# Kernel tuning notes

Measured on AMD Instinct MI355X. Metric: run time of the kernel, lower is better.

The kernel has to match this reference:

```python
import jax, jax.numpy as jnp
import numpy as np

# Grid of blocks: blocks[i][j] is Linear(D, D) if mask[i, j] else None.
N_OUT, N_IN, D, B = 8, 8, 128, 32768
BAND = 2  # active blocks: j <= i and i - j <= BAND


def setup_inputs() -> dict:
    key = jax.random.key(0)
    k1, k2, k3 = jax.random.split(key, 3)
    # X: (num input blocks, batch, block feature dim)
    X = jax.random.normal(k1, (N_IN, B, D), dtype=jnp.float32)
    # W[i, j]: torch.nn.Linear weight of block (i, j), shape (out, in)
    W = jax.random.normal(k2, (N_OUT, N_IN, D, D), dtype=jnp.float32) / np.sqrt(D).astype(np.float32)
    b = jax.random.normal(k3, (N_OUT, N_IN, D), dtype=jnp.float32) * 0.01
    i = jnp.arange(N_OUT)[:, None]
    j = jnp.arange(N_IN)[None, :]
    mask = (j <= i) & (i - j <= BAND)  # banded lower-triangular block sparsity
    return {"X": X, "W": W, "b": b, "mask": mask}


def reference(X, W, b, mask):
    # Sequential2D forward: out[i] = sum_j (X[j] @ W[i,j].T + b[i,j]) over active blocks.
    # None blocks contribute a zero vector, which we express by zeroing masked weights/biases.
    m = mask.astype(W.dtype)                       # (i, j)
    Wm = W * m[:, :, None, None]                   # zero out None blocks
    out = jnp.einsum('jbd,ijod->ibo', X, Wm)       # block-row summation of Linear outputs
    bias = jnp.sum(b * m[:, :, None], axis=1)      # (i, o): sum of active biases per row
    return out + bias[:, None, :]                  # (num_out_blocks, batch, block_out)
```

## Files before the change

kernel.cpp:

```cpp
#include <hip/hip_runtime.h>


#define NOUT  8
#define NIN   8
#define DD    128
#define BATCH 32768
#define BAND  2

#define BM    128
#define WROWS 32
#define SKW   136

typedef __attribute__((ext_vector_type(8))) short  short8;
typedef __attribute__((ext_vector_type(4))) float  floatx4;

__device__ __forceinline__ unsigned short f2bf(float f) {
    unsigned int u = __float_as_uint(f);
    u += 0x7fffu + ((u >> 16) & 1u);
    return (unsigned short)(u >> 16);
}

__device__ __forceinline__ short8 pack8(floatx4 f0, floatx4 f1) {
    short8 p;
    p[0] = (short)f2bf(f0[0]); p[1] = (short)f2bf(f0[1]);
    p[2] = (short)f2bf(f0[2]); p[3] = (short)f2bf(f0[3]);
    p[4] = (short)f2bf(f1[0]); p[5] = (short)f2bf(f1[1]);
    p[6] = (short)f2bf(f1[2]); p[7] = (short)f2bf(f1[3]);
    return p;
}

__global__ __launch_bounds__(256, 2)
void seq2d_kernel(const float* __restrict__ X,
                  const float* __restrict__ W,
                  const float* __restrict__ Bv,
                  float* __restrict__ out) {
    const int i  = blockIdx.y;
    const int m0 = blockIdx.x * BM;

    __shared__ unsigned short sW[DD * SKW];
    __shared__ float sbias[DD];

    const int tid  = threadIdx.x;
    const int lane = tid & 63;
    const int wave = tid >> 6;
    const int l15  = lane & 15;
    const int quad = lane >> 4;
    const int wrow = wave * WROWS;

    int jlo = i - BAND; if (jlo < 0) jlo = 0;
    const int ncs = (i - jlo + 1) * 4;

    const float* xb = X + (size_t)(m0 + wrow + l15) * DD + quad * 8;

    floatx4 px[4][2][2];

    auto prefetch = [&](int slot, int c) {
        const int j  = jlo + (c >> 2);
        const int k0 = (c & 3) * 32;
        const float* p = xb + (size_t)j * (BATCH * DD) + k0;
        px[slot][0][0] = *(const floatx4*)(p);
        px[slot][0][1] = *(const floatx4*)(p + 4);
        px[slot][1][0] = *(const floatx4*)(p + 16 * DD);
        px[slot][1][1] = *(const floatx4*)(p + 16 * DD + 4);
    };

    prefetch(0, 0);
    prefetch(1, 1);
    prefetch(2, 2);
    prefetch(3, 3);

    if (tid < DD) {
        float s = 0.f;
        for (int j = jlo; j <= i; ++j)
            s += Bv[(i * NIN + j) * DD + tid];
        sbias[tid] = s;
    }

    floatx4 acc[2][8];
#pragma unroll
    for (int a = 0; a < 2; ++a)
#pragma unroll
        for (int n = 0; n < 8; ++n)
            acc[a][n] = (floatx4){0.f, 0.f, 0.f, 0.f};

    const int wr_r = tid >> 3;
    const int wr_c = (tid & 7) << 4;

    int c = 0;
    for (int j = jlo; j <= i; ++j) {
        const float* wsrc = W + (size_t)(i * NIN + j) * DD * DD;
        __syncthreads();
#pragma unroll
        for (int p = 0; p < 4; ++p) {
            const int r = p * 32 + wr_r;
            const float* wp = wsrc + (size_t)r * DD + wr_c;
            floatx4 w0 = *(const floatx4*)(wp);
            floatx4 w1 = *(const floatx4*)(wp + 4);
            floatx4 w2 = *(const floatx4*)(wp + 8);
            floatx4 w3 = *(const floatx4*)(wp + 12);
            *(short8*)&sW[r * SKW + wr_c]     = pack8(w0, w1);
            *(short8*)&sW[r * SKW + wr_c + 8] = pack8(w2, w3);
        }
        __syncthreads();

#pragma unroll
        for (int ks = 0; ks < 4; ++ks) {
            short8 a0 = pack8(px[ks][0][0], px[ks][0][1]);
            short8 a1 = pack8(px[ks][1][0], px[ks][1][1]);
            if (c + 4 < ncs) prefetch(ks, c + 4);

#pragma unroll
            for (int nf = 0; nf < 8; ++nf) {
                short8 bfrag = *(const short8*)&sW[(nf * 16 + l15) * SKW + ks * 32 + quad * 8];
                acc[0][nf] = __builtin_amdgcn_mfma_f32_16x16x32_bf16(a0, bfrag, acc[0][nf], 0, 0, 0);
                acc[1][nf] = __builtin_amdgcn_mfma_f32_16x16x32_bf16(a1, bfrag, acc[1][nf], 0, 0, 0);
            }
            ++c;
        }
    }

    float* outi = out + (size_t)i * BATCH * DD;
#pragma unroll
    for (int mf = 0; mf < 2; ++mf) {
#pragma unroll
        for (int nf = 0; nf < 8; ++nf) {
            const int n_g  = nf * 16 + l15;
            const float bs = sbias[n_g];
            const int m_b  = m0 + wrow + mf * 16 + quad * 4;
#pragma unroll
            for (int r = 0; r < 4; ++r)
                __builtin_nontemporal_store(acc[mf][nf][r] + bs,
                                            &outi[(size_t)(m_b + r) * DD + n_g]);
        }
    }
}

extern "C" void kernel_launch(void* const* d_in, const int* in_sizes, int n_in,
                              void* d_out, int out_size, void* d_ws, size_t ws_size,
                              hipStream_t stream) {
    const float* X  = (const float*)d_in[0];
    const float* W  = (const float*)d_in[1];
    const float* Bv = (const float*)d_in[2];
    float* out = (float*)d_out;

    dim3 grid(BATCH / BM, NOUT);
    seq2d_kernel<<<grid, 256, 0, stream>>>(X, W, Bv, out);
}
```

Before: 283.3 us.

## Use 512-thread blocks with one 16-row M fragment per wave and custom barriers

Doubles the workgroup to 8 waves so each wave owns a single 16-row slice, which halves the per-thread accumulator and prefetch registers and targets higher occupancy (launch bounds 512,4). Each thread now loads one 32-float weight row segment per j, replacing the 4-pass loop. __syncthreads is replaced by raw s_barrier plus sched_barrier and an explicit lgkmcnt wait, so the barrier does not drain outstanding global prefetches. Output stores switch from nontemporal to plain stores. The trade-off is that each B fragment read from LDS now feeds only one MFMA instead of two, so LDS traffic per MFMA doubles.

Result: no change. 288.2 us (+1.7%).

```diff
diff --git a/kernel.cpp b/kernel.cpp
--- a/kernel.cpp
+++ b/kernel.cpp
@@ -8,7 +8,6 @@
 #define BAND  2
 
 #define BM    128
-#define WROWS 32
 #define SKW   136
 
 typedef __attribute__((ext_vector_type(8))) short  short8;
@@ -29,7 +28,13 @@
     return p;
 }
 
-__global__ __launch_bounds__(256, 2)
+__device__ __forceinline__ void barrier_nodrain() {
+    __builtin_amdgcn_sched_barrier(0);
+    __builtin_amdgcn_s_barrier();
+    __builtin_amdgcn_sched_barrier(0);
+}
+
+__global__ __launch_bounds__(512, 4)
 void seq2d_kernel(const float* __restrict__ X,
                   const float* __restrict__ W,
                   const float* __restrict__ Bv,
@@ -45,23 +50,20 @@
     const int wave = tid >> 6;
     const int l15  = lane & 15;
     const int quad = lane >> 4;
-    const int wrow = wave * WROWS;
 
     int jlo = i - BAND; if (jlo < 0) jlo = 0;
     const int ncs = (i - jlo + 1) * 4;
 
-    const float* xb = X + (size_t)(m0 + wrow + l15) * DD + quad * 8;
+    const float* xb = X + (size_t)(m0 + wave * 16 + l15) * DD + quad * 8;
 
-    floatx4 px[4][2][2];
+    floatx4 px[4][2];
 
     auto prefetch = [&](int slot, int c) {
         const int j  = jlo + (c >> 2);
         const int k0 = (c & 3) * 32;
         const float* p = xb + (size_t)j * (BATCH * DD) + k0;
-        px[slot][0][0] = *(const floatx4*)(p);
-        px[slot][0][1] = *(const floatx4*)(p + 4);
-        px[slot][1][0] = *(const floatx4*)(p + 16 * DD);
-        px[slot][1][1] = *(const floatx4*)(p + 16 * DD + 4);
+        px[slot][0] = *(const floatx4*)(p);
+        px[slot][1] = *(const floatx4*)(p + 4);
     };
 
     prefetch(0, 0);
@@ -76,62 +78,64 @@
         sbias[tid] = s;
     }
 
-    floatx4 acc[2][8];
+    floatx4 acc[8];
 #pragma unroll
-    for (int a = 0; a < 2; ++a)
-#pragma unroll
-        for (int n = 0; n < 8; ++n)
-            acc[a][n] = (floatx4){0.f, 0.f, 0.f, 0.f};
+    for (int n = 0; n < 8; ++n)
+        acc[n] = (floatx4){0.f, 0.f, 0.f, 0.f};
 
-    const int wr_r = tid >> 3;
-    const int wr_c = (tid & 7) << 4;
+    const int wr_r = tid >> 2;
+    const int wr_c = (tid & 3) << 5;
 
     int c = 0;
     for (int j = jlo; j <= i; ++j) {
-        const float* wsrc = W + (size_t)(i * NIN + j) * DD * DD;
-        __syncthreads();
-#pragma unroll
-        for (int p = 0; p < 4; ++p) {
-            const int r = p * 32 + wr_r;
-            const float* wp = wsrc + (size_t)r * DD + wr_c;
-            floatx4 w0 = *(const floatx4*)(wp);
-            floatx4 w1 = *(const floatx4*)(wp + 4);
-            floatx4 w2 = *(const floatx4*)(wp + 8);
-            floatx4 w3 = *(const floatx4*)(wp + 12);
-            *(short8*)&sW[r * SKW + wr_c]     = pack8(w0, w1);
-            *(short8*)&sW[r * SKW + wr_c + 8] = pack8(w2, w3);
+        const float* wsrc = W + (size_t)(i * NIN + j) * DD * DD
+                              + (size_t)wr_r * DD + wr_c;
+
+        barrier_nodrain();
+
+        {
+            floatx4 w0 = *(const floatx4*)(wsrc);
+            floatx4 w1 = *(const floatx4*)(wsrc + 4);
+            floatx4 w2 = *(const floatx4*)(wsrc + 8);
+            floatx4 w3 = *(const floatx4*)(wsrc + 12);
+            *(short8*)&sW[wr_r * SKW + wr_c]     = pack8(w0, w1);
+            *(short8*)&sW[wr_r * SKW + wr_c + 8] = pack8(w2, w3);
         }
-        __syncthreads();
+        {
+            floatx4 w4 = *(const floatx4*)(wsrc + 16);
+            floatx4 w5 = *(const floatx4*)(wsrc + 20);
+            floatx4 w6 = *(const floatx4*)(wsrc + 24);
+            floatx4 w7 = *(const floatx4*)(wsrc + 28);
+            *(short8*)&sW[wr_r * SKW + wr_c + 16] = pack8(w4, w5);
+            *(short8*)&sW[wr_r * SKW + wr_c + 24] = pack8(w6, w7);
+        }
+
+        asm volatile("s_waitcnt lgkmcnt(0)" ::: "memory");
+        barrier_nodrain();
 
 #pragma unroll
         for (int ks = 0; ks < 4; ++ks) {
-            short8 a0 = pack8(px[ks][0][0], px[ks][0][1]);
-            short8 a1 = pack8(px[ks][1][0], px[ks][1][1]);
+            short8 a = pack8(px[ks][0], px[ks][1]);
             if (c + 4 < ncs) prefetch(ks, c + 4);
 
 #pragma unroll
             for (int nf = 0; nf < 8; ++nf) {
                 short8 bfrag = *(const short8*)&sW[(nf * 16 + l15) * SKW + ks * 32 + quad * 8];
-                acc[0][nf] = __builtin_amdgcn_mfma_f32_16x16x32_bf16(a0, bfrag, acc[0][nf], 0, 0, 0);
-                acc[1][nf] = __builtin_amdgcn_mfma_f32_16x16x32_bf16(a1, bfrag, acc[1][nf], 0, 0, 0);
+                acc[nf] = __builtin_amdgcn_mfma_f32_16x16x32_bf16(a, bfrag, acc[nf], 0, 0, 0);
             }
             ++c;
         }
     }
 
     float* outi = out + (size_t)i * BATCH * DD;
+    const int m_b = m0 + wave * 16 + quad * 4;
 #pragma unroll
-    for (int mf = 0; mf < 2; ++mf) {
+    for (int nf = 0; nf < 8; ++nf) {
+        const int n_g  = nf * 16 + l15;
+        const float bs = sbias[n_g];
 #pragma unroll
-        for (int nf = 0; nf < 8; ++nf) {
-            const int n_g  = nf * 16 + l15;
-            const float bs = sbias[n_g];
-            const int m_b  = m0 + wrow + mf * 16 + quad * 4;
-#pragma unroll
-            for (int r = 0; r < 4; ++r)
-                __builtin_nontemporal_store(acc[mf][nf][r] + bs,
-                                            &outi[(size_t)(m_b + r) * DD + n_g]);
-        }
+        for (int r = 0; r < 4; ++r)
+            outi[(size_t)(m_b + r) * DD + n_g] = acc[nf][r] + bs;
     }
 }
 
@@ -144,5 +148,5 @@
     float* out = (float*)d_out;
 
     dim3 grid(BATCH / BM, NOUT);
-    seq2d_kernel<<<grid, 256, 0, stream>>>(X, W, Bv, out);
+    seq2d_kernel<<<grid, 512, 0, stream>>>(X, W, Bv, out);
 }
```

## Preload all weight blocks into registers and pipeline X loads with explicit waitcnt

Applied to the files above, without the earlier changes.

The banded weight blocks for each output row are now all loaded and converted to bf16 up front: the first goes into LDS and the rest are held in registers, then restaged into LDS between phases. This removes global weight loads from the main loop. X prefetches are issued through inline asm with hand-placed vmcnt waits, so four k-steps of loads stay in flight across block boundaries. The LDS layout drops padding in favour of an XOR swizzle, and output stores become normal instead of nontemporal. The costs are higher register pressure from holding up to two extra weight blocks, and fragile hand-tuned wait counts.

Measured after the change: 313.0 us. 1.1x slower.

```diff
diff --git a/kernel.cpp b/kernel.cpp
--- a/kernel.cpp
+++ b/kernel.cpp
@@ -6,10 +6,8 @@
 #define DD    128
 #define BATCH 32768
 #define BAND  2
-
 #define BM    128
-#define WROWS 32
-#define SKW   136
+#define XSTRIDE ((size_t)BATCH * DD)
 
 typedef __attribute__((ext_vector_type(8))) short  short8;
 typedef __attribute__((ext_vector_type(4))) float  floatx4;
@@ -29,6 +27,50 @@
     return p;
 }
 
+#define KSTEP(ks, WAITN, PNEXT, REISSUE)                                        \
+  {                                                                             \
+    asm volatile("s_waitcnt vmcnt(" #WAITN ")");                                \
+    __builtin_amdgcn_sched_barrier(0);                                          \
+    short8 a0 = pack8(px[ks][0][0], px[ks][0][1]);                              \
+    short8 a1 = pack8(px[ks][1][0], px[ks][1][1]);                              \
+    if (REISSUE) {                                                              \
+      const float* p_ = (PNEXT) + (ks) * 32;                                    \
+      asm volatile("global_load_dwordx4 %0, %4, off\n\t"                        \
+                   "global_load_dwordx4 %1, %4, off offset:16\n\t"              \
+                   "global_load_dwordx4 %2, %5, off\n\t"                        \
+                   "global_load_dwordx4 %3, %5, off offset:16"                  \
+                   : "=&v"(px[ks][0][0]), "=&v"(px[ks][0][1]),                  \
+                     "=&v"(px[ks][1][0]), "=&v"(px[ks][1][1])                   \
+                   : "v"(p_), "v"(p_ + 16 * DD));                               \
+    }                                                                           \
+    _Pragma("unroll")                                                           \
+    for (int nf = 0; nf < 8; ++nf) {                                            \
+      const short8 bfrag = *(const short8*)                                     \
+          &sW[(nf * 16 + l15) * 128 + ((((ks) * 4 + quad) ^ l15) << 3)];        \
+      acc[0][nf] = __builtin_amdgcn_mfma_f32_16x16x32_bf16(a0, bfrag, acc[0][nf], 0, 0, 0); \
+      acc[1][nf] = __builtin_amdgcn_mfma_f32_16x16x32_bf16(a1, bfrag, acc[1][nf], 0, 0, 0); \
+    }                                                                           \
+  }
+
+#define PHASE_MID(PN)  { KSTEP(0,12,PN,1) KSTEP(1,12,PN,1) KSTEP(2,12,PN,1) KSTEP(3,12,PN,1) }
+#define PHASE_LAST()   { KSTEP(0,12,xb,0) KSTEP(1, 8,xb,0) KSTEP(2, 4,xb,0) KSTEP(3, 0,xb,0) }
+
+#define RESTAGE(WREGS)                                                          \
+  {                                                                             \
+    __builtin_amdgcn_sched_barrier(0);                                          \
+    __builtin_amdgcn_s_barrier();                                               \
+    __builtin_amdgcn_sched_barrier(0);                                          \
+    unsigned short* sb_ = &sW[wr_r * 128];                                      \
+    _Pragma("unroll")                                                           \
+    for (int w_ = 0; w_ < 8; ++w_)                                              \
+      *(short8*)&sb_[(((wr_cb0 + w_) ^ (wr_r & 15)) << 3)] = WREGS[w_];         \
+    __builtin_amdgcn_sched_barrier(0);                                          \
+    asm volatile("s_waitcnt lgkmcnt(0)");                                       \
+    __builtin_amdgcn_sched_barrier(0);                                          \
+    __builtin_amdgcn_s_barrier();                                               \
+    __builtin_amdgcn_sched_barrier(0);                                          \
+  }
+
 __global__ __launch_bounds__(256, 2)
 void seq2d_kernel(const float* __restrict__ X,
                   const float* __restrict__ W,
@@ -37,7 +79,7 @@
     const int i  = blockIdx.y;
     const int m0 = blockIdx.x * BM;
 
-    __shared__ unsigned short sW[DD * SKW];
+    __shared__ unsigned short sW[DD * 128];
     __shared__ float sbias[DD];
 
     const int tid  = threadIdx.x;
@@ -45,29 +87,21 @@
     const int wave = tid >> 6;
     const int l15  = lane & 15;
     const int quad = lane >> 4;
-    const int wrow = wave * WROWS;
 
     int jlo = i - BAND; if (jlo < 0) jlo = 0;
-    const int ncs = (i - jlo + 1) * 4;
-
-    const float* xb = X + (size_t)(m0 + wrow + l15) * DD + quad * 8;
+    const int nj = i - jlo + 1;
+
+    const float* xb = X + (size_t)(m0 + wave * 32 + l15) * DD + quad * 8;
 
     floatx4 px[4][2][2];
-
-    auto prefetch = [&](int slot, int c) {
-        const int j  = jlo + (c >> 2);
-        const int k0 = (c & 3) * 32;
-        const float* p = xb + (size_t)j * (BATCH * DD) + k0;
-        px[slot][0][0] = *(const floatx4*)(p);
-        px[slot][0][1] = *(const floatx4*)(p + 4);
-        px[slot][1][0] = *(const floatx4*)(p + 16 * DD);
-        px[slot][1][1] = *(const floatx4*)(p + 16 * DD + 4);
-    };
-
-    prefetch(0, 0);
-    prefetch(1, 1);
-    prefetch(2, 2);
-    prefetch(3, 3);
+#pragma unroll
+    for (int ks = 0; ks < 4; ++ks) {
+        const float* p = xb + (size_t)jlo * XSTRIDE + ks * 32;
+        px[ks][0][0] = *(const floatx4*)(p);
+        px[ks][0][1] = *(const floatx4*)(p + 4);
+        px[ks][1][0] = *(const floatx4*)(p + 16 * DD);
+        px[ks][1][1] = *(const floatx4*)(p + 16 * DD + 4);
+    }
 
     if (tid < DD) {
         float s = 0.f;
@@ -76,6 +110,45 @@
         sbias[tid] = s;
     }
 
+    const int wr_r   = tid >> 1;
+    const int wr_cb0 = (tid & 1) * 8;
+
+    {
+        const float* ws = W + (size_t)(i * NIN + jlo) * DD * DD
+                            + (size_t)wr_r * DD + wr_cb0 * 8;
+        unsigned short* sb = &sW[wr_r * 128];
+#pragma unroll
+        for (int w = 0; w < 8; ++w) {
+            floatx4 a = *(const floatx4*)(ws + w * 8);
+            floatx4 b = *(const floatx4*)(ws + w * 8 + 4);
+            *(short8*)&sb[(((wr_cb0 + w) ^ (wr_r & 15)) << 3)] = pack8(a, b);
+        }
+    }
+
+    short8 w1s[8], w2s[8];
+    if (nj >= 2) {
+        const float* ws = W + (size_t)(i * NIN + jlo + 1) * DD * DD
+                            + (size_t)wr_r * DD + wr_cb0 * 8;
+#pragma unroll
+        for (int w = 0; w < 8; ++w) {
+            floatx4 a = *(const floatx4*)(ws + w * 8);
+            floatx4 b = *(const floatx4*)(ws + w * 8 + 4);
+            w1s[w] = pack8(a, b);
+        }
+    }
+    if (nj >= 3) {
+        const float* ws = W + (size_t)(i * NIN + jlo + 2) * DD * DD
+                            + (size_t)wr_r * DD + wr_cb0 * 8;
+#pragma unroll
+        for (int w = 0; w < 8; ++w) {
+            floatx4 a = *(const floatx4*)(ws + w * 8);
+            floatx4 b = *(const floatx4*)(ws + w * 8 + 4);
+            w2s[w] = pack8(a, b);
+        }
+    }
+
+    __syncthreads();
+
     floatx4 acc[2][8];
 #pragma unroll
     for (int a = 0; a < 2; ++a)
@@ -83,54 +156,34 @@
         for (int n = 0; n < 8; ++n)
             acc[a][n] = (floatx4){0.f, 0.f, 0.f, 0.f};
 
-    const int wr_r = tid >> 3;
-    const int wr_c = (tid & 7) << 4;
-
-    int c = 0;
-    for (int j = jlo; j <= i; ++j) {
-        const float* wsrc = W + (size_t)(i * NIN + j) * DD * DD;
-        __syncthreads();
-#pragma unroll
-        for (int p = 0; p < 4; ++p) {
-            const int r = p * 32 + wr_r;
-            const float* wp = wsrc + (size_t)r * DD + wr_c;
-            floatx4 w0 = *(const floatx4*)(wp);
-            floatx4 w1 = *(const floatx4*)(wp + 4);
-            floatx4 w2 = *(const floatx4*)(wp + 8);
-            floatx4 w3 = *(const floatx4*)(wp + 12);
-            *(short8*)&sW[r * SKW + wr_c]     = pack8(w0, w1);
-            *(short8*)&sW[r * SKW + wr_c + 8] = pack8(w2, w3);
-        }
-        __syncthreads();
-
-#pragma unroll
-        for (int ks = 0; ks < 4; ++ks) {
-            short8 a0 = pack8(px[ks][0][0], px[ks][0][1]);
-            short8 a1 = pack8(px[ks][1][0], px[ks][1][1]);
-            if (c + 4 < ncs) prefetch(ks, c + 4);
-
-#pragma unroll
-            for (int nf = 0; nf < 8; ++nf) {
-                short8 bfrag = *(const short8*)&sW[(nf * 16 + l15) * SKW + ks * 32 + quad * 8];
-                acc[0][nf] = __builtin_amdgcn_mfma_f32_16x16x32_bf16(a0, bfrag, acc[0][nf], 0, 0, 0);
-                acc[1][nf] = __builtin_amdgcn_mfma_f32_16x16x32_bf16(a1, bfrag, acc[1][nf], 0, 0, 0);
-            }
-            ++c;
-        }
+    if (nj == 1) {
+        PHASE_LAST();
+    } else if (nj == 2) {
+        const float* p1 = xb + (size_t)(jlo + 1) * XSTRIDE;
+        PHASE_MID(p1);
+        RESTAGE(w1s);
+        PHASE_LAST();
+    } else {
+        const float* p1 = xb + (size_t)(jlo + 1) * XSTRIDE;
+        const float* p2 = xb + (size_t)(jlo + 2) * XSTRIDE;
+        PHASE_MID(p1);
+        RESTAGE(w1s);
+        PHASE_MID(p2);
+        RESTAGE(w2s);
+        PHASE_LAST();
     }
 
     float* outi = out + (size_t)i * BATCH * DD;
 #pragma unroll
     for (int mf = 0; mf < 2; ++mf) {
+        const int m_b = m0 + wave * 32 + mf * 16 + quad * 4;
 #pragma unroll
         for (int nf = 0; nf < 8; ++nf) {
             const int n_g  = nf * 16 + l15;
             const float bs = sbias[n_g];
-            const int m_b  = m0 + wrow + mf * 16 + quad * 4;
 #pragma unroll
             for (int r = 0; r < 4; ++r)
-                __builtin_nontemporal_store(acc[mf][nf][r] + bs,
-                                            &outi[(size_t)(m_b + r) * DD + n_g]);
+                outi[(size_t)(m_b + r) * DD + n_g] = acc[mf][nf][r] + bs;
         }
     }
 }
```

## Stage X tiles through swizzled LDS and coalesce output stores via LDS

Applied to the files above, without the earlier changes.

Replaces the per-lane strided register prefetch of X with cooperative, fully coalesced loads that are converted to bf16 and written into an XOR-swizzled LDS tile. The weight tile uses the same swizzle, and the padded layout is dropped. Results are staged in LDS and written out as contiguous float4 stores. The aim is better global-memory coalescing and fewer LDS bank conflicts. In exchange it loses the register prefetch overlap, adds extra barriers per block, and raises LDS use to about 64KB, which may hurt occupancy.

Result: slower. 363.2 us (+28.2%).

```diff
diff --git a/kernel.cpp b/kernel.cpp
--- a/kernel.cpp
+++ b/kernel.cpp
@@ -6,27 +6,16 @@
 #define DD    128
 #define BATCH 32768
 #define BAND  2
-
 #define BM    128
-#define WROWS 32
-#define SKW   136
 
 typedef __attribute__((ext_vector_type(8))) short  short8;
+typedef __attribute__((ext_vector_type(4))) short  bf16x4;
 typedef __attribute__((ext_vector_type(4))) float  floatx4;
 
 __device__ __forceinline__ unsigned short f2bf(float f) {
     unsigned int u = __float_as_uint(f);
     u += 0x7fffu + ((u >> 16) & 1u);
     return (unsigned short)(u >> 16);
-}
-
-__device__ __forceinline__ short8 pack8(floatx4 f0, floatx4 f1) {
-    short8 p;
-    p[0] = (short)f2bf(f0[0]); p[1] = (short)f2bf(f0[1]);
-    p[2] = (short)f2bf(f0[2]); p[3] = (short)f2bf(f0[3]);
-    p[4] = (short)f2bf(f1[0]); p[5] = (short)f2bf(f1[1]);
-    p[6] = (short)f2bf(f1[2]); p[7] = (short)f2bf(f1[3]);
-    return p;
 }
 
 __global__ __launch_bounds__(256, 2)
@@ -37,37 +26,19 @@
     const int i  = blockIdx.y;
     const int m0 = blockIdx.x * BM;
 
-    __shared__ unsigned short sW[DD * SKW];
+    __shared__ unsigned short sU[2 * DD * DD];
     __shared__ float sbias[DD];
+
+    unsigned short* sX = sU;
+    unsigned short* sW = sU + DD * DD;
 
     const int tid  = threadIdx.x;
     const int lane = tid & 63;
     const int wave = tid >> 6;
     const int l15  = lane & 15;
     const int quad = lane >> 4;
-    const int wrow = wave * WROWS;
 
     int jlo = i - BAND; if (jlo < 0) jlo = 0;
-    const int ncs = (i - jlo + 1) * 4;
-
-    const float* xb = X + (size_t)(m0 + wrow + l15) * DD + quad * 8;
-
-    floatx4 px[4][2][2];
-
-    auto prefetch = [&](int slot, int c) {
-        const int j  = jlo + (c >> 2);
-        const int k0 = (c & 3) * 32;
-        const float* p = xb + (size_t)j * (BATCH * DD) + k0;
-        px[slot][0][0] = *(const floatx4*)(p);
-        px[slot][0][1] = *(const floatx4*)(p + 4);
-        px[slot][1][0] = *(const floatx4*)(p + 16 * DD);
-        px[slot][1][1] = *(const floatx4*)(p + 16 * DD + 4);
-    };
-
-    prefetch(0, 0);
-    prefetch(1, 1);
-    prefetch(2, 2);
-    prefetch(3, 3);
 
     if (tid < DD) {
         float s = 0.f;
@@ -76,6 +47,21 @@
         sbias[tid] = s;
     }
 
+    auto stage = [&](const float* __restrict__ gsrc, unsigned short* __restrict__ sdst) {
+#pragma unroll
+        for (int q = 0; q < 16; ++q) {
+            const int fi  = q * 1024 + tid * 4;
+            floatx4 v = *(const floatx4*)(gsrc + fi);
+            const int row = fi >> 7;
+            const int col = fi & 127;
+            const int pu  = (col >> 3) ^ (row & 15);
+            bf16x4 pk;
+            pk[0] = (short)f2bf(v[0]); pk[1] = (short)f2bf(v[1]);
+            pk[2] = (short)f2bf(v[2]); pk[3] = (short)f2bf(v[3]);
+            *(bf16x4*)&sdst[row * 128 + (pu << 3) + (col & 7)] = pk;
+        }
+    };
+
     floatx4 acc[2][8];
 #pragma unroll
     for (int a = 0; a < 2; ++a)
@@ -83,55 +69,46 @@
         for (int n = 0; n < 8; ++n)
             acc[a][n] = (floatx4){0.f, 0.f, 0.f, 0.f};
 
-    const int wr_r = tid >> 3;
-    const int wr_c = (tid & 7) << 4;
-
-    int c = 0;
     for (int j = jlo; j <= i; ++j) {
-        const float* wsrc = W + (size_t)(i * NIN + j) * DD * DD;
-        __syncthreads();
-#pragma unroll
-        for (int p = 0; p < 4; ++p) {
-            const int r = p * 32 + wr_r;
-            const float* wp = wsrc + (size_t)r * DD + wr_c;
-            floatx4 w0 = *(const floatx4*)(wp);
-            floatx4 w1 = *(const floatx4*)(wp + 4);
-            floatx4 w2 = *(const floatx4*)(wp + 8);
-            floatx4 w3 = *(const floatx4*)(wp + 12);
-            *(short8*)&sW[r * SKW + wr_c]     = pack8(w0, w1);
-            *(short8*)&sW[r * SKW + wr_c + 8] = pack8(w2, w3);
-        }
+        stage(X + (size_t)j * (BATCH * DD) + (size_t)m0 * DD, sX);
+        stage(W + (size_t)(i * NIN + j) * DD * DD, sW);
         __syncthreads();
 
 #pragma unroll
         for (int ks = 0; ks < 4; ++ks) {
-            short8 a0 = pack8(px[ks][0][0], px[ks][0][1]);
-            short8 a1 = pack8(px[ks][1][0], px[ks][1][1]);
-            if (c + 4 < ncs) prefetch(ks, c + 4);
-
+            const int ku = (((ks * 4 + quad) ^ l15) << 3);
+            short8 a0 = *(const short8*)&sX[(wave * 32 +  0 + l15) * 128 + ku];
+            short8 a1 = *(const short8*)&sX[(wave * 32 + 16 + l15) * 128 + ku];
 #pragma unroll
             for (int nf = 0; nf < 8; ++nf) {
-                short8 bfrag = *(const short8*)&sW[(nf * 16 + l15) * SKW + ks * 32 + quad * 8];
+                short8 bfrag = *(const short8*)&sW[(nf * 16 + l15) * 128 + ku];
                 acc[0][nf] = __builtin_amdgcn_mfma_f32_16x16x32_bf16(a0, bfrag, acc[0][nf], 0, 0, 0);
                 acc[1][nf] = __builtin_amdgcn_mfma_f32_16x16x32_bf16(a1, bfrag, acc[1][nf], 0, 0, 0);
             }
-            ++c;
         }
+        __syncthreads();
     }
 
-    float* outi = out + (size_t)i * BATCH * DD;
+    float* sO = (float*)sU;
 #pragma unroll
     for (int mf = 0; mf < 2; ++mf) {
+        const int r0 = wave * 32 + mf * 16 + quad * 4;
 #pragma unroll
         for (int nf = 0; nf < 8; ++nf) {
             const int n_g  = nf * 16 + l15;
             const float bs = sbias[n_g];
-            const int m_b  = m0 + wrow + mf * 16 + quad * 4;
 #pragma unroll
             for (int r = 0; r < 4; ++r)
-                __builtin_nontemporal_store(acc[mf][nf][r] + bs,
-                                            &outi[(size_t)(m_b + r) * DD + n_g]);
+                sO[(r0 + r) * DD + n_g] = acc[mf][nf][r] + bs;
         }
+    }
+    __syncthreads();
+
+    float* od = out + (size_t)i * (BATCH * DD) + (size_t)m0 * DD;
+#pragma unroll
+    for (int q = 0; q < 16; ++q) {
+        const int fi = q * 1024 + tid * 4;
+        *(floatx4*)(od + fi) = *(const floatx4*)&sO[fi];
     }
 }
 
```
